# Kernel tuning notes

Measured on AMD Instinct MI355X. Metric: run time of the kernel, lower is better.

The kernel has to match this reference:

```python
import jax, jax.numpy as jnp
import numpy as np

N_NODES = 100000
N_EDGES = 1000000
IN_FEAT = 64
OUT_FEAT = 64


def setup_inputs() -> dict:
    key = jax.random.key(0)
    ks = jax.random.split(key, 12)
    d, o = IN_FEAT, OUT_FEAT
    s = 1.0 / np.sqrt(d)
    s2 = 1.0 / np.sqrt(2 * d)
    return {
        "x": jax.random.normal(ks[0], (N_NODES, d), dtype=jnp.float32),
        "edge_index": jax.random.randint(ks[1], (2, N_EDGES), 0, N_NODES, dtype=jnp.int64),
        "batch": jnp.zeros((N_NODES,), dtype=jnp.int64),
        # message MLP: Linear(d,d) -> ReLU -> Linear(d,d)
        "msg_w1": jax.random.uniform(ks[2], (d, d), jnp.float32, -s, s),
        "msg_b1": jax.random.uniform(ks[3], (d,), jnp.float32, -s, s),
        "msg_w2": jax.random.uniform(ks[4], (d, d), jnp.float32, -s, s),
        "msg_b2": jax.random.uniform(ks[5], (d,), jnp.float32, -s, s),
        # output MLP: Linear(2d,d) -> ReLU -> Linear(d,out)
        "out_w1": jax.random.uniform(ks[6], (2 * d, d), jnp.float32, -s2, s2),
        "out_b1": jax.random.uniform(ks[7], (d,), jnp.float32, -s2, s2),
        "out_w2": jax.random.uniform(ks[8], (d, o), jnp.float32, -s, s),
        "out_b2": jax.random.uniform(ks[9], (o,), jnp.float32, -s, s),
    }


def reference(x, edge_index, batch, msg_w1, msg_b1, msg_w2, msg_b2,
              out_w1, out_b1, out_w2, out_b2):
    row, col = edge_index[0], edge_index[1]
    # gather source-node features per edge, apply message MLP
    h = x[row]                                   # [E, d]
    msg = jax.nn.relu(h @ msg_w1 + msg_b1) @ msg_w2 + msg_b2  # [E, d]
    # force processor: node features pass through as fx; scatter-sum messages
    fx = x                                        # [N, d]
    agg = jax.ops.segment_sum(msg, col, num_segments=N_NODES)  # [N, d]
    out_final = jnp.concatenate([fx, agg], axis=1)  # [N, 2d]
    out = jax.nn.relu(out_final @ out_w1 + out_b1) @ out_w2 + out_b2  # [N, out]
    return out
```

## Files before the change

### kernel.cpp

```cpp
#include <hip/hip_runtime.h>
#include <hip/hip_bf16.h>

#define D 64
#define BSHIFT 6
#define BW (1 << BSHIFT)
#define MAXB 2048
#define CAP 4096
#define STRIDE 2048
#define GT 256
#define SMEM_BYTES 27648

typedef __attribute__((ext_vector_type(8))) short bf16x8;
typedef __attribute__((ext_vector_type(4))) float f32x4;

__device__ __forceinline__ short f2bf(float f) {
    __hip_bfloat16 h = __float2bfloat16(f);
    return *reinterpret_cast<short*>(&h);
}

__global__ __launch_bounds__(256) void msg_bin_kernel(
    const float* __restrict__ x,
    const float* __restrict__ w1, const float* __restrict__ b1,
    const float* __restrict__ w2, const float* __restrict__ b2,
    __hip_bfloat16* __restrict__ m, int n_nodes,
    const int* __restrict__ row, const int* __restrict__ col,
    int* __restrict__ gcur, unsigned int* __restrict__ tmp,
    int n_edges, int nbuckets, int chunk, int nmsg)
{
    __shared__ __align__(16) char smem[SMEM_BYTES];

    if ((int)blockIdx.x >= nmsg) {
        int* hist = (int*)smem;
        int* base = hist + MAXB;
        int* lcur = base + MAXB;
        const int t = threadIdx.x;
        const int bb = blockIdx.x - nmsg;
        const int e0 = bb * chunk;
        const int e1 = min(e0 + chunk, n_edges);

        for (int i = t; i < nbuckets; i += 256) hist[i] = 0;
        __syncthreads();
        for (int e = e0 + t; e < e1; e += 256)
            atomicAdd(&hist[col[e] >> BSHIFT], 1);
        __syncthreads();
        for (int i = t; i < nbuckets; i += 256) {
            base[i] = hist[i] ? atomicAdd(&gcur[i], hist[i]) : 0;
            lcur[i] = 0;
        }
        __syncthreads();
        for (int e = e0 + t; e < e1; e += 256) {
            int c = col[e];
            int b = c >> BSHIFT;
            int loc = base[b] + atomicAdd(&lcur[b], 1);
            if (loc < STRIDE) {
                unsigned int val = ((unsigned int)(c & (BW - 1)) << 17)
                                 | (unsigned int)row[e];
                tmp[(size_t)b * STRIDE + loc] = val;
            }
        }
        return;
    }

    __hip_bfloat16* sHb = (__hip_bfloat16*)smem;
    short* sW1 = (short*)(smem + 9216);
    short* sW2 = (short*)(smem + 18432);

    const int tid  = threadIdx.x;
    const int lane = tid & 63;
    const int wslot = tid >> 6;
    const int mr   = lane & 15;
    const int quad = lane >> 4;

    for (int i = tid; i < 1024; i += 256) {
        const int r = i >> 4, c = (i & 15) * 4;
        float4 f = *(const float4*)&w1[i * 4];
        short* d = &sW1[r * 72 + c];
        d[0] = f2bf(f.x); d[1] = f2bf(f.y); d[2] = f2bf(f.z); d[3] = f2bf(f.w);
        float4 g = *(const float4*)&w2[i * 4];
        short* e = &sW2[r * 72 + c];
        e[0] = f2bf(g.x); e[1] = f2bf(g.y); e[2] = f2bf(g.z); e[3] = f2bf(g.w);
    }
    __syncthreads();

    bf16x8 w1f[2][4], w2f[2][4];
    float  b1v[4], b2v[4];
#pragma unroll
    for (int ks = 0; ks < 2; ++ks)
#pragma unroll
        for (int nb = 0; nb < 4; ++nb) {
            bf16x8 f1, f2;
#pragma unroll
            for (int j = 0; j < 8; ++j) {
                int k = ks * 32 + quad * 8 + j;
                f1[j] = sW1[k * 72 + nb * 16 + mr];
                f2[j] = sW2[k * 72 + nb * 16 + mr];
            }
            w1f[ks][nb] = f1;
            w2f[ks][nb] = f2;
        }
#pragma unroll
    for (int nb = 0; nb < 4; ++nb) {
        b1v[nb] = b1[nb * 16 + mr];
        b2v[nb] = b2[nb * 16 + mr];
    }

    __hip_bfloat16* Hw = sHb + wslot * (16 * 72);
    const int wid    = (blockIdx.x * 256 + threadIdx.x) >> 6;
    const int nwaves = nmsg * 4;
    const int ntiles = (n_nodes + 15) >> 4;

    for (int t = wid; t < ntiles; t += nwaves) {
        const int v0 = t * 16;
        int vr = v0 + mr;
        if (vr >= n_nodes) vr = n_nodes - 1;

        bf16x8 a[2];
#pragma unroll
        for (int ks = 0; ks < 2; ++ks) {
            const float* p = x + (size_t)vr * D + ks * 32 + quad * 8;
            float4 lo = *(const float4*)p;
            float4 hi = *(const float4*)(p + 4);
            bf16x8 f;
            f[0] = f2bf(lo.x); f[1] = f2bf(lo.y); f[2] = f2bf(lo.z); f[3] = f2bf(lo.w);
            f[4] = f2bf(hi.x); f[5] = f2bf(hi.y); f[6] = f2bf(hi.z); f[7] = f2bf(hi.w);
            a[ks] = f;
        }

#pragma unroll
        for (int nb = 0; nb < 4; ++nb) {
            f32x4 acc = {0.f, 0.f, 0.f, 0.f};
            acc = __builtin_amdgcn_mfma_f32_16x16x32_bf16(a[0], w1f[0][nb], acc, 0, 0, 0);
            acc = __builtin_amdgcn_mfma_f32_16x16x32_bf16(a[1], w1f[1][nb], acc, 0, 0, 0);
#pragma unroll
            for (int r = 0; r < 4; ++r) {
                float hv = fmaxf(acc[r] + b1v[nb], 0.f);
                Hw[(quad * 4 + r) * 72 + nb * 16 + mr] = __float2bfloat16(hv);
            }
        }

        bf16x8 h[2];
#pragma unroll
        for (int ks = 0; ks < 2; ++ks)
            h[ks] = *(const bf16x8*)&Hw[mr * 72 + ks * 32 + quad * 8];

#pragma unroll
        for (int nb = 0; nb < 4; ++nb) {
            f32x4 acc = {0.f, 0.f, 0.f, 0.f};
            acc = __builtin_amdgcn_mfma_f32_16x16x32_bf16(h[0], w2f[0][nb], acc, 0, 0, 0);
            acc = __builtin_amdgcn_mfma_f32_16x16x32_bf16(h[1], w2f[1][nb], acc, 0, 0, 0);
#pragma unroll
            for (int r = 0; r < 4; ++r)
                Hw[(quad * 4 + r) * 72 + nb * 16 + mr] =
                    __float2bfloat16(acc[r] + b2v[nb]);
        }

#pragma unroll
        for (int s = 0; s < 2; ++s) {
            const int rrow = s * 8 + (lane >> 3);
            const int cblk = (lane & 7) * 8;
            bf16x8 val = *(const bf16x8*)&Hw[rrow * 72 + cblk];
            const int vrow = v0 + rrow;
            if (vrow < n_nodes)
                *(bf16x8*)&m[(size_t)vrow * D + cblk] = val;
        }
    }
}

__global__ __launch_bounds__(GT) void bucket_gather_kernel(
    const int* __restrict__ gcur, const unsigned int* __restrict__ tmp,
    const __hip_bfloat16* __restrict__ m, __hip_bfloat16* __restrict__ agg,
    int n_nodes, int nbuckets)
{
    __shared__ unsigned int sorted[CAP];
    __shared__ int cnt[BW], off[BW], cur[BW];

    const int b    = blockIdx.x;
    const int t    = threadIdx.x;
    const int lane = t & 63;
    const int wv   = t >> 6;
    const int vbase = b << BSHIFT;
    const unsigned int* gtmp = tmp + (size_t)b * STRIDE;

    const int total = min(gcur[b], STRIDE);

    float acc[16];
#pragma unroll
    for (int i = 0; i < 16; ++i) acc[i] = 0.f;

    for (int r0 = 0; r0 < total; r0 += CAP) {
        const int r1 = min(r0 + CAP, total);

        if (t < BW) cnt[t] = 0;
        __syncthreads();

        for (int i = r0 + t; i < r1; i += GT)
            atomicAdd(&cnt[gtmp[i] >> 17], 1);
        __syncthreads();

        if (wv == 0) {
            int a0 = cnt[lane];
            int s0 = a0;
#pragma unroll
            for (int d = 1; d < 64; d <<= 1) {
                int u0 = __shfl_up(s0, d, 64);
                if (lane >= d) s0 += u0;
            }
            const int e0 = s0 - a0;
            off[lane] = e0;
            cur[lane] = e0;
        }
        __syncthreads();

        for (int i = r0 + t; i < r1; i += GT) {
            unsigned int u = gtmp[i];
            int pos = atomicAdd(&cur[u >> 17], 1);
            sorted[pos] = u;
        }
        __syncthreads();

#pragma unroll
        for (int i = 0; i < 16; ++i) {
            const int n  = wv + (i << 2);
            const int o0 = off[n];
            const int c  = cnt[n];
            float s = 0.f;
            for (int cs = 0; cs < c; cs += 64) {
                const int k = min(64, c - cs);
                unsigned int pv = 0;
                if (lane < k) pv = sorted[o0 + cs + lane];

                int j = 0;
                for (; j + 8 <= k; j += 8) {
                    unsigned int u[8];
                    float v[8];
#pragma unroll
                    for (int q = 0; q < 8; ++q)
                        u[q] = __builtin_amdgcn_readlane(pv, j + q);
#pragma unroll
                    for (int q = 0; q < 8; ++q)
                        v[q] = (float)m[(size_t)(u[q] & 0x1FFFFu) * D + lane];
#pragma unroll
                    for (int q = 0; q < 8; ++q)
                        s += v[q];
                }
                for (; j < k; ++j) {
                    unsigned int u = __builtin_amdgcn_readlane(pv, j);
                    s += (float)m[(size_t)(u & 0x1FFFFu) * D + lane];
                }
            }
            acc[i] += s;
        }
        if (r1 < total) __syncthreads();
    }

#pragma unroll
    for (int i = 0; i < 16; ++i) {
        const int v = vbase + wv + (i << 2);
        if (v < n_nodes)
            agg[(size_t)v * D + lane] = __float2bfloat16(acc[i]);
    }
}

__global__ __launch_bounds__(256) void scatter_kernel(
    const int* __restrict__ row, const int* __restrict__ col,
    const __hip_bfloat16* __restrict__ m, float* __restrict__ aggf, int n_edges)
{
    const int lane = threadIdx.x & 63;
    const int wid  = (blockIdx.x * blockDim.x + threadIdx.x) >> 6;
    const int base = wid * 64;
    if (base >= n_edges) return;
    const int cnt = min(64, n_edges - base);

    int my_r = 0, my_c = 0;
    if (lane < cnt) { my_r = row[base + lane]; my_c = col[base + lane]; }

    for (int j = 0; j < cnt; ++j) {
        int r = __builtin_amdgcn_readlane(my_r, j);
        int c = __builtin_amdgcn_readlane(my_c, j);
        float v = (float)m[(size_t)r * D + lane];
        atomicAdd(&aggf[(size_t)c * D + lane], v);
    }
}

__global__ __launch_bounds__(256) void cvt_kernel(
    const float* __restrict__ aggf, __hip_bfloat16* __restrict__ agg, int n)
{
    int i = blockIdx.x * blockDim.x + threadIdx.x;
    if (i < n) agg[i] = __float2bfloat16(aggf[i]);
}

__global__ __launch_bounds__(256) void out_kernel(
    const float* __restrict__ x, const __hip_bfloat16* __restrict__ agg,
    const float* __restrict__ w1, const float* __restrict__ b1,
    const float* __restrict__ w2, const float* __restrict__ b2,
    float* __restrict__ out, int n_nodes)
{
    __shared__ __align__(16) __hip_bfloat16 sH[4][16 * 72];
    __shared__ short sW1[128 * 72];
    __shared__ short sW2[64 * 72];

    const int tid  = threadIdx.x;
    const int lane = tid & 63;
    const int wslot = tid >> 6;
    const int mr   = lane & 15;
    const int quad = lane >> 4;

    for (int i = tid; i < 2048; i += 256) {
        const int r = i >> 4, c = (i & 15) * 4;
        float4 f = *(const float4*)&w1[i * 4];
        short* d = &sW1[r * 72 + c];
        d[0] = f2bf(f.x); d[1] = f2bf(f.y); d[2] = f2bf(f.z); d[3] = f2bf(f.w);
    }
    for (int i = tid; i < 1024; i += 256) {
        const int r = i >> 4, c = (i & 15) * 4;
        float4 g = *(const float4*)&w2[i * 4];
        short* e = &sW2[r * 72 + c];
        e[0] = f2bf(g.x); e[1] = f2bf(g.y); e[2] = f2bf(g.z); e[3] = f2bf(g.w);
    }
    __syncthreads();

    bf16x8 w1f[4][4], w2f[2][4];
    float  b1v[4], b2v[4];
#pragma unroll
    for (int ks = 0; ks < 4; ++ks)
#pragma unroll
        for (int nb = 0; nb < 4; ++nb) {
            bf16x8 f;
#pragma unroll
            for (int j = 0; j < 8; ++j) {
                int k = ks * 32 + quad * 8 + j;
                f[j] = sW1[k * 72 + nb * 16 + mr];
            }
            w1f[ks][nb] = f;
        }
#pragma unroll
    for (int ks = 0; ks < 2; ++ks)
#pragma unroll
        for (int nb = 0; nb < 4; ++nb) {
            bf16x8 f;
#pragma unroll
            for (int j = 0; j < 8; ++j) {
                int k = ks * 32 + quad * 8 + j;
                f[j] = sW2[k * 72 + nb * 16 + mr];
            }
            w2f[ks][nb] = f;
        }
#pragma unroll
    for (int nb = 0; nb < 4; ++nb) {
        b1v[nb] = b1[nb * 16 + mr];
        b2v[nb] = b2[nb * 16 + mr];
    }

    __hip_bfloat16* Hw = sH[wslot];
    const int wid    = (blockIdx.x * blockDim.x + threadIdx.x) >> 6;
    const int nwaves = (gridDim.x * blockDim.x) >> 6;
    const int ntiles = (n_nodes + 15) >> 4;

    for (int t = wid; t < ntiles; t += nwaves) {
        const int v0 = t * 16;
        int vr = v0 + mr;
        if (vr >= n_nodes) vr = n_nodes - 1;

        bf16x8 a[4];
#pragma unroll
        for (int ks = 0; ks < 2; ++ks) {
            const float* p = x + (size_t)vr * D + ks * 32 + quad * 8;
            float4 lo = *(const float4*)p;
            float4 hi = *(const float4*)(p + 4);
            bf16x8 f;
            f[0] = f2bf(lo.x); f[1] = f2bf(lo.y); f[2] = f2bf(lo.z); f[3] = f2bf(lo.w);
            f[4] = f2bf(hi.x); f[5] = f2bf(hi.y); f[6] = f2bf(hi.z); f[7] = f2bf(hi.w);
            a[ks] = f;
        }
#pragma unroll
        for (int ks = 2; ks < 4; ++ks)
            a[ks] = *(const bf16x8*)&agg[(size_t)vr * D + (ks - 2) * 32 + quad * 8];

#pragma unroll
        for (int nb = 0; nb < 4; ++nb) {
            f32x4 acc = {0.f, 0.f, 0.f, 0.f};
#pragma unroll
            for (int ks = 0; ks < 4; ++ks)
                acc = __builtin_amdgcn_mfma_f32_16x16x32_bf16(a[ks], w1f[ks][nb], acc, 0, 0, 0);
#pragma unroll
            for (int r = 0; r < 4; ++r) {
                float hv = fmaxf(acc[r] + b1v[nb], 0.f);
                Hw[(quad * 4 + r) * 72 + nb * 16 + mr] = __float2bfloat16(hv);
            }
        }

        bf16x8 h[2];
#pragma unroll
        for (int ks = 0; ks < 2; ++ks)
            h[ks] = *(const bf16x8*)&Hw[mr * 72 + ks * 32 + quad * 8];

#pragma unroll
        for (int nb = 0; nb < 4; ++nb) {
            f32x4 acc = {0.f, 0.f, 0.f, 0.f};
            acc = __builtin_amdgcn_mfma_f32_16x16x32_bf16(h[0], w2f[0][nb], acc, 0, 0, 0);
            acc = __builtin_amdgcn_mfma_f32_16x16x32_bf16(h[1], w2f[1][nb], acc, 0, 0, 0);
#pragma unroll
            for (int r = 0; r < 4; ++r) {
                int vrow = v0 + quad * 4 + r;
                if (vrow < n_nodes)
                    out[(size_t)vrow * D + nb * 16 + mr] = acc[r] + b2v[nb];
            }
        }
    }
}

extern "C" void kernel_launch(void* const* d_in, const int* in_sizes, int n_in,
                              void* d_out, int out_size, void* d_ws, size_t ws_size,
                              hipStream_t stream) {
    const float* x   = (const float*)d_in[0];
    const int*   ei  = (const int*)d_in[1];
    const float* mw1 = (const float*)d_in[3];
    const float* mb1 = (const float*)d_in[4];
    const float* mw2 = (const float*)d_in[5];
    const float* mb2 = (const float*)d_in[6];
    const float* ow1 = (const float*)d_in[7];
    const float* ob1 = (const float*)d_in[8];
    const float* ow2 = (const float*)d_in[9];
    const float* ob2 = (const float*)d_in[10];

    const int n_nodes = in_sizes[0] / D;
    const int n_edges = in_sizes[1] / 2;
    const int* row = ei;
    const int* col = ei + n_edges;

    const int nbuckets = (n_nodes + BW - 1) >> BSHIFT;

    __hip_bfloat16* m   = (__hip_bfloat16*)d_ws;
    __hip_bfloat16* agg = m + (size_t)n_nodes * D;
    unsigned int* tmp   = (unsigned int*)(agg + (size_t)n_nodes * D);
    const size_t region = (size_t)nbuckets * STRIDE * 4 > (size_t)n_nodes * D * 4
                        ? (size_t)nbuckets * STRIDE * 4 : (size_t)n_nodes * D * 4;
    int* gcur = (int*)((char*)tmp + region);
    float* aggf = (float*)tmp;
    const size_t need = (size_t)n_nodes * D * 4 + region + (size_t)nbuckets * 4;

    const int ntiles = (n_nodes + 15) / 16;
    int nmsg = (ntiles + 3) / 4;
    if (nmsg > 512) nmsg = 512;

    const bool shape_ok = (n_nodes < (1 << 17)) && (nbuckets <= MAXB)
                       && (n_edges <= nbuckets * (STRIDE / 2));

    if (ws_size >= need && shape_ok) {
        hipMemsetAsync(gcur, 0, (size_t)nbuckets * sizeof(int), stream);
        const int nbbin = 256;
        const int chunk = (n_edges + nbbin - 1) / nbbin;
        msg_bin_kernel<<<nmsg + nbbin, 256, 0, stream>>>(
            x, mw1, mb1, mw2, mb2, m, n_nodes,
            row, col, gcur, tmp, n_edges, nbuckets, chunk, nmsg);
        bucket_gather_kernel<<<nbuckets, GT, 0, stream>>>(gcur, tmp, m, agg,
                                                          n_nodes, nbuckets);
    } else {
        msg_bin_kernel<<<nmsg, 256, 0, stream>>>(
            x, mw1, mb1, mw2, mb2, m, n_nodes,
            row, col, gcur, tmp, n_edges, nbuckets, 0, nmsg);
        hipMemsetAsync(aggf, 0, (size_t)n_nodes * D * sizeof(float), stream);
        const int nwaves_s = (n_edges + 63) / 64;
        scatter_kernel<<<(nwaves_s + 3) / 4, 256, 0, stream>>>(row, col, m, aggf, n_edges);
        cvt_kernel<<<((n_nodes * D) + 255) / 256, 256, 0, stream>>>(aggf, agg, n_nodes * D);
    }

    out_kernel<<<nmsg, 256, 0, stream>>>(x, agg, ow1, ob1, ow2, ob2,
                                         (float*)d_out, n_nodes);
}
```

Baseline: 181.7 us.

## Fuse output MLP into bucket gather kernel with precomputed bf16 weight fragments

Folds the output MLP into the bucket-gather kernel. Each block now keeps its aggregated 64-node tile in shared memory and runs both MFMA layers directly, so the bf16 agg tensor is no longer written and read back and one launch is removed. One extra block in the message/bin kernel pre-packs the output weights into MFMA-ready bf16 fragments in workspace. In exchange the gather kernel uses more registers and shared memory, and it re-reads x inside the gather stage.

After: 196.6 us. 8.2% more time.

```diff
diff --git a/kernel.cpp b/kernel.cpp
--- a/kernel.cpp
+++ b/kernel.cpp
@@ -9,6 +9,7 @@
 #define STRIDE 2048
 #define GT 256
 #define SMEM_BYTES 27648
+#define WFRAG_SHORTS (24 * 64 * 8)
 
 typedef __attribute__((ext_vector_type(8))) short bf16x8;
 typedef __attribute__((ext_vector_type(4))) float f32x4;
@@ -25,9 +26,30 @@
     __hip_bfloat16* __restrict__ m, int n_nodes,
     const int* __restrict__ row, const int* __restrict__ col,
     int* __restrict__ gcur, unsigned int* __restrict__ tmp,
-    int n_edges, int nbuckets, int chunk, int nmsg)
+    int n_edges, int nbuckets, int chunk, int nmsg, int nbin,
+    const float* __restrict__ ow1, const float* __restrict__ ow2,
+    short* __restrict__ wfrag)
 {
     __shared__ __align__(16) char smem[SMEM_BYTES];
+
+    if ((int)blockIdx.x >= nmsg + nbin) {
+        const int t = threadIdx.x;
+        for (int idx = t; idx < 24 * 64; idx += 256) {
+            const int f = idx >> 6;
+            const int l = idx & 63;
+            const int mrL = l & 15, quadL = l >> 4;
+            const float* w; int ks, nb;
+            if (f < 16) { ks = f >> 2;        nb = f & 3;        w = ow1; }
+            else        { ks = (f - 16) >> 2; nb = (f - 16) & 3; w = ow2; }
+            short* dst = wfrag + (size_t)idx * 8;
+#pragma unroll
+            for (int j = 0; j < 8; ++j) {
+                const int k = ks * 32 + quadL * 8 + j;
+                dst[j] = f2bf(w[k * D + nb * 16 + mrL]);
+            }
+        }
+        return;
+    }
 
     if ((int)blockIdx.x >= nmsg) {
         int* hist = (int*)smem;
@@ -166,13 +188,16 @@
     }
 }
 
-__global__ __launch_bounds__(GT) void bucket_gather_kernel(
+__global__ __launch_bounds__(GT) void bucket_gather_out_kernel(
     const int* __restrict__ gcur, const unsigned int* __restrict__ tmp,
-    const __hip_bfloat16* __restrict__ m, __hip_bfloat16* __restrict__ agg,
-    int n_nodes, int nbuckets)
+    const __hip_bfloat16* __restrict__ m, const float* __restrict__ x,
+    const short* __restrict__ wfrag,
+    const float* __restrict__ ob1, const float* __restrict__ ob2,
+    float* __restrict__ out, int n_nodes, int nbuckets)
 {
-    __shared__ unsigned int sorted[CAP];
+    __shared__ __align__(16) char smem[18432];
     __shared__ int cnt[BW], off[BW], cur[BW];
+    unsigned int* sorted = (unsigned int*)smem;
 
     const int b    = blockIdx.x;
     const int t    = threadIdx.x;
@@ -250,14 +275,80 @@
             }
             acc[i] += s;
         }
-        if (r1 < total) __syncthreads();
-    }
-
-#pragma unroll
-    for (int i = 0; i < 16; ++i) {
-        const int v = vbase + wv + (i << 2);
-        if (v < n_nodes)
-            agg[(size_t)v * D + lane] = __float2bfloat16(acc[i]);
+        __syncthreads();
+    }
+
+    __hip_bfloat16* aggT = (__hip_bfloat16*)smem;
+    __hip_bfloat16* sH   = (__hip_bfloat16*)(smem + 9216);
+
+#pragma unroll
+    for (int i = 0; i < 16; ++i)
+        aggT[(wv + (i << 2)) * 72 + lane] = __float2bfloat16(acc[i]);
+    __syncthreads();
+
+    const int mr   = lane & 15;
+    const int quad = lane >> 4;
+    const int v0   = vbase + wv * 16;
+    int vr = v0 + mr;
+    if (vr >= n_nodes) vr = n_nodes - 1;
+
+    bf16x8 a[4];
+#pragma unroll
+    for (int ks = 0; ks < 2; ++ks) {
+        const float* p = x + (size_t)vr * D + ks * 32 + quad * 8;
+        float4 lo = *(const float4*)p;
+        float4 hi = *(const float4*)(p + 4);
+        bf16x8 f;
+        f[0] = f2bf(lo.x); f[1] = f2bf(lo.y); f[2] = f2bf(lo.z); f[3] = f2bf(lo.w);
+        f[4] = f2bf(hi.x); f[5] = f2bf(hi.y); f[6] = f2bf(hi.z); f[7] = f2bf(hi.w);
+        a[ks] = f;
+    }
+#pragma unroll
+    for (int ks = 2; ks < 4; ++ks)
+        a[ks] = *(const bf16x8*)&aggT[(wv * 16 + mr) * 72 + (ks - 2) * 32 + quad * 8];
+
+    float b1v[4], b2v[4];
+#pragma unroll
+    for (int nb = 0; nb < 4; ++nb) {
+        b1v[nb] = ob1[nb * 16 + mr];
+        b2v[nb] = ob2[nb * 16 + mr];
+    }
+
+    __hip_bfloat16* Hw = sH + wv * (16 * 72);
+#pragma unroll
+    for (int nb = 0; nb < 4; ++nb) {
+        f32x4 c4 = {0.f, 0.f, 0.f, 0.f};
+#pragma unroll
+        for (int ks = 0; ks < 4; ++ks) {
+            bf16x8 wf = *(const bf16x8*)&wfrag[((size_t)(ks * 4 + nb) * 64 + lane) * 8];
+            c4 = __builtin_amdgcn_mfma_f32_16x16x32_bf16(a[ks], wf, c4, 0, 0, 0);
+        }
+#pragma unroll
+        for (int r = 0; r < 4; ++r) {
+            float hv = fmaxf(c4[r] + b1v[nb], 0.f);
+            Hw[(quad * 4 + r) * 72 + nb * 16 + mr] = __float2bfloat16(hv);
+        }
+    }
+
+    bf16x8 h[2];
+#pragma unroll
+    for (int ks = 0; ks < 2; ++ks)
+        h[ks] = *(const bf16x8*)&Hw[mr * 72 + ks * 32 + quad * 8];
+
+#pragma unroll
+    for (int nb = 0; nb < 4; ++nb) {
+        f32x4 c4 = {0.f, 0.f, 0.f, 0.f};
+#pragma unroll
+        for (int ks = 0; ks < 2; ++ks) {
+            bf16x8 wf = *(const bf16x8*)&wfrag[((size_t)(16 + ks * 4 + nb) * 64 + lane) * 8];
+            c4 = __builtin_amdgcn_mfma_f32_16x16x32_bf16(h[ks], wf, c4, 0, 0, 0);
+        }
+#pragma unroll
+        for (int r = 0; r < 4; ++r) {
+            const int vrow = v0 + quad * 4 + r;
+            if (vrow < n_nodes)
+                out[(size_t)vrow * D + nb * 16 + mr] = c4[r] + b2v[nb];
+        }
     }
 }
 
@@ -436,8 +527,9 @@
     const size_t region = (size_t)nbuckets * STRIDE * 4 > (size_t)n_nodes * D * 4
                         ? (size_t)nbuckets * STRIDE * 4 : (size_t)n_nodes * D * 4;
     int* gcur = (int*)((char*)tmp + region);
+    short* wfrag = (short*)(((size_t)(char*)(gcur + nbuckets) + 15) & ~(size_t)15);
     float* aggf = (float*)tmp;
-    const size_t need = (size_t)n_nodes * D * 4 + region + (size_t)nbuckets * 4;
+    const size_t need = (size_t)((char*)(wfrag + WFRAG_SHORTS) - (char*)d_ws);
 
     const int ntiles = (n_nodes + 15) / 16;
     int nmsg = (ntiles + 3) / 4;
@@ -450,21 +542,22 @@
         hipMemsetAsync(gcur, 0, (size_t)nbuckets * sizeof(int), stream);
         const int nbbin = 256;
         const int chunk = (n_edges + nbbin - 1) / nbbin;
-        msg_bin_kernel<<<nmsg + nbbin, 256, 0, stream>>>(
+        msg_bin_kernel<<<nmsg + nbbin + 1, 256, 0, stream>>>(
             x, mw1, mb1, mw2, mb2, m, n_nodes,
-            row, col, gcur, tmp, n_edges, nbuckets, chunk, nmsg);
-        bucket_gather_kernel<<<nbuckets, GT, 0, stream>>>(gcur, tmp, m, agg,
-                                                          n_nodes, nbuckets);
+            row, col, gcur, tmp, n_edges, nbuckets, chunk, nmsg, nbbin,
+            ow1, ow2, wfrag);
+        bucket_gather_out_kernel<<<nbuckets, GT, 0, stream>>>(
+            gcur, tmp, m, x, wfrag, ob1, ob2, (float*)d_out, n_nodes, nbuckets);
     } else {
         msg_bin_kernel<<<nmsg, 256, 0, stream>>>(
             x, mw1, mb1, mw2, mb2, m, n_nodes,
-            row, col, gcur, tmp, n_edges, nbuckets, 0, nmsg);
+            row, col, gcur, tmp, n_edges, nbuckets, 0, nmsg, 0,
+            ow1, ow2, (short*)agg );
         hipMemsetAsync(aggf, 0, (size_t)n_nodes * D * sizeof(float), stream);
         const int nwaves_s = (n_edges + 63) / 64;
         scatter_kernel<<<(nwaves_s + 3) / 4, 256, 0, stream>>>(row, col, m, aggf, n_edges);
         cvt_kernel<<<((n_nodes * D) + 255) / 256, 256, 0, stream>>>(aggf, agg, n_nodes * D);
-    }
-
-    out_kernel<<<nmsg, 256, 0, stream>>>(x, agg, ow1, ob1, ow2, ob2,
-                                         (float*)d_out, n_nodes);
-}
+        out_kernel<<<nmsg, 256, 0, stream>>>(x, agg, ow1, ob1, ow2, ob2,
+                                             (float*)d_out, n_nodes);
+    }
+}
```
